# Kernel optimization log

Measured on AMD Instinct MI355X. Metric: run time of the kernel, lower is better.

## Reference

```python
import jax, jax.numpy as jnp
import numpy as np

L, N, EMB, H = 4, 50000, 128, 4
R, HID, LBL = 16, 64, 32
E = 625000


def setup_inputs() -> dict:
    key = jax.random.key(0)
    ks = jax.random.split(key, 10)
    s = 0.05
    return {
        "embedding": jax.random.normal(ks[0], (L, N, EMB), jnp.float32),
        "in_proj_w": jax.random.normal(ks[1], (3 * EMB, EMB), jnp.float32) * s,
        "in_proj_b": jnp.zeros((3 * EMB,), jnp.float32),
        "out_proj_w": jax.random.normal(ks[2], (EMB, EMB), jnp.float32) * s,
        "out_proj_b": jnp.zeros((EMB,), jnp.float32),
        "w1": jax.random.normal(ks[3], (R, EMB, HID), jnp.float32) * s,
        "root1": jax.random.normal(ks[4], (EMB, HID), jnp.float32) * s,
        "b1": jnp.zeros((HID,), jnp.float32),
        "w2": jax.random.normal(ks[5], (R, HID, LBL), jnp.float32) * s,
        "root2": jax.random.normal(ks[6], (HID, LBL), jnp.float32) * s,
        "b2": jnp.zeros((LBL,), jnp.float32),
        "edge_index": jax.random.randint(ks[7], (2, E), 0, N, dtype=jnp.int64),
        "edge_type": jax.random.randint(ks[8], (E,), 0, R, dtype=jnp.int64),
    }


def mha_self(x, wi, bi, wo, bo):
    # x: (L, N, EMB) -- torch nn.MultiheadAttention, batch_first=False, q=k=v=x
    Ls, Ns, Es = x.shape
    hd = Es // H
    qkv = x @ wi.T + bi                      # (L, N, 3E)
    q, k, v = jnp.split(qkv, 3, axis=-1)
    q = q.reshape(Ls, Ns, H, hd)
    k = k.reshape(Ls, Ns, H, hd)
    v = v.reshape(Ls, Ns, H, hd)
    scores = jnp.einsum('lnhd,mnhd->nhlm', q, k) / np.sqrt(hd).astype(np.float32)
    attn = jax.nn.softmax(scores, axis=-1)
    out = jnp.einsum('nhlm,mnhd->lnhd', attn, v).reshape(Ls, Ns, Es)
    return out @ wo.T + bo


def rgcn_layer(x, src, dst, etype, W, root, bias):
    # PyG RGCNConv (num_bases=None, aggr='mean'):
    # out[n] = x[n] @ root + bias + sum_r mean_{e: dst=n, type=r} x[src_e] @ W[r]
    Rr, fin, fout = W.shape
    seg = etype * N + dst                                   # (E,) combined (rel, dst)
    msg_sum = jax.ops.segment_sum(x[src], seg, num_segments=Rr * N)   # (R*N, fin)
    cnt = jax.ops.segment_sum(jnp.ones((src.shape[0],), x.dtype), seg,
                              num_segments=Rr * N)
    mean = (msg_sum / jnp.maximum(cnt, 1.0)[:, None]).reshape(Rr, N, fin)
    agg = jnp.einsum('rni,rio->no', mean, W)                # per-relation GEMM
    return agg + x @ root + bias


def reference(embedding, in_proj_w, in_proj_b, out_proj_w, out_proj_b,
              w1, root1, b1, w2, root2, b2, edge_index, edge_type):
    attn_out = mha_self(embedding, in_proj_w, in_proj_b, out_proj_w, out_proj_b)
    x = attn_out[0]                                         # (N, EMB)
    src, dst = edge_index[0], edge_index[1]
    x = jax.nn.relu(rgcn_layer(x, src, dst, edge_type, w1, root1, b1))
    x = rgcn_layer(x, src, dst, edge_type, w2, root2, b2)
    return jax.nn.softmax(x, axis=-1)
```

## Files before the change

### kernel.cpp

```cpp
#include <hip/hip_runtime.h>
#include <hip/hip_bf16.h>
#include <math.h>

#define NNODES 50000
#define NEDGE 625000
#define RREL 16
#define SCAN_NB 196

typedef __attribute__((ext_vector_type(8))) short short8;
typedef __attribute__((ext_vector_type(4))) float f32x4;

__device__ __forceinline__ float bfu(ushort u) {
  return __uint_as_float(((unsigned)u) << 16);
}
__device__ __forceinline__ ushort f2b(float f) {
  __hip_bfloat16 h = __float2bfloat16(f);
  return *(ushort*)&h;
}

__global__ __launch_bounds__(256) void prep_weights(
    const float* __restrict__ ipw, const float* __restrict__ opw,
    const float* __restrict__ w1, const float* __restrict__ root1,
    const float* __restrict__ w2, const float* __restrict__ root2,
    __hip_bfloat16* __restrict__ BTqkv, __hip_bfloat16* __restrict__ BTout,
    __hip_bfloat16* __restrict__ BT1, __hip_bfloat16* __restrict__ BT2) {
  int i = blockIdx.x * 256 + threadIdx.x;
  if (i < 49152) {
    BTqkv[i] = __float2bfloat16(ipw[i]);
  } else if (i < 65536) {
    int j = i - 49152;
    BTout[j] = __float2bfloat16(opw[j]);
  } else if (i < 65536 + 139264) {
    int j = i - 65536; int c = j / 128, k = j % 128;
    float v;
    if (c < 64) v = root1[k * 64 + c];
    else { int r = (c - 64) >> 6, o = (c - 64) & 63; v = w1[r * 8192 + k * 64 + o]; }
    BT1[j] = __float2bfloat16(v);
  } else if (i < 65536 + 139264 + 34816) {
    int j = i - 65536 - 139264; int c = j / 64, k = j % 64;
    float v;
    if (c < 32) v = root2[k * 32 + c];
    else { int r = (c - 32) >> 5, o = (c - 32) & 31; v = w2[r * 2048 + k * 32 + o]; }
    BT2[j] = __float2bfloat16(v);
  }
}

__global__ __launch_bounds__(256) void qkv_gemm(
    const float* __restrict__ A, const __hip_bfloat16* __restrict__ BT,
    const float* __restrict__ bias, __hip_bfloat16* __restrict__ C) {
  __shared__ ushort As[128 * 128];
  __shared__ ushort Cs[128 * 136];
  const int t = threadIdx.x;
  const long row0 = (long)blockIdx.x * 128;

#pragma unroll
  for (int c = t; c < 128 * 16; c += 256) {
    int r = c >> 4, cc = c & 15;
    long gm = row0 + r;
    int4 v = make_int4(0, 0, 0, 0);
    if (gm < 200000) {
      const float* ap = A + gm * 128 + cc * 8;
      float4 f0 = *(const float4*)ap;
      float4 f1 = *(const float4*)(ap + 4);
      v.x = (int)f2b(f0.x) | ((int)f2b(f0.y) << 16);
      v.y = (int)f2b(f0.z) | ((int)f2b(f0.w) << 16);
      v.z = (int)f2b(f1.x) | ((int)f2b(f1.y) << 16);
      v.w = (int)f2b(f1.z) | ((int)f2b(f1.w) << 16);
    }
    *(int4*)(As + r * 128 + ((cc ^ (r & 7)) * 8)) = v;
  }
  __syncthreads();

  const int lane = t & 63, w = t >> 6;
  const int wr = (w >> 1) * 64, wc = (w & 1) * 64;
  const int lrow = lane & 15, lk = lane >> 4;
  const int nstrips = (row0 < NNODES) ? 3 : 2;

  for (int s = 0; s < nstrips; s++) {
    const int col0 = (s == 2) ? 0 : 128 + s * 128;
    const long Meff = (s == 2) ? NNODES : 200000;

    const ushort* bp[4];
#pragma unroll
    for (int j = 0; j < 4; j++)
      bp[j] = (const ushort*)BT + (long)(col0 + wc + j * 16 + lrow) * 128 + lk * 8;

    f32x4 acc[4][4];
#pragma unroll
    for (int i = 0; i < 4; i++)
#pragma unroll
      for (int j = 0; j < 4; j++) acc[i][j] = (f32x4){0.f, 0.f, 0.f, 0.f};

#pragma unroll
    for (int k0 = 0; k0 < 128; k0 += 32) {
      const int cb = k0 / 8 + lk;
      short8 af[4], bfr[4];
#pragma unroll
      for (int j = 0; j < 4; j++) bfr[j] = *(const short8*)(bp[j] + k0);
#pragma unroll
      for (int i = 0; i < 4; i++) {
        int ra = wr + i * 16 + lrow;
        af[i] = *(const short8*)(As + ra * 128 + ((cb ^ (ra & 7)) * 8));
      }
#pragma unroll
      for (int i = 0; i < 4; i++)
#pragma unroll
        for (int j = 0; j < 4; j++)
          acc[i][j] = __builtin_amdgcn_mfma_f32_16x16x32_bf16(af[i], bfr[j], acc[i][j], 0, 0, 0);
    }

    __syncthreads();
#pragma unroll
    for (int j = 0; j < 4; j++) {
      int coll = wc + j * 16 + lrow;
      float bv = bias[col0 + coll];
#pragma unroll
      for (int i = 0; i < 4; i++) {
        int rbase = wr + i * 16 + lk * 4;
#pragma unroll
        for (int q = 0; q < 4; q++)
          Cs[(rbase + q) * 136 + coll] = f2b(acc[i][j][q] + bv);
      }
    }
    __syncthreads();
#pragma unroll
    for (int idx = t; idx < 128 * 16; idx += 256) {
      int r = idx >> 4, k = idx & 15;
      long gm = row0 + r;
      if (gm < Meff)
        *(int4*)((ushort*)C + gm * 384 + col0 + k * 8) = *(const int4*)(Cs + r * 136 + k * 8);
    }
  }
}

template <int K, bool AF32>
__global__ __launch_bounds__(256) void gemm_mfma(
    const void* __restrict__ Av, const __hip_bfloat16* __restrict__ BT,
    const float* __restrict__ bias, __hip_bfloat16* __restrict__ C,
    int M, int N, int lda, int ldc) {
  constexpr int CPR = K / 8;
  __shared__ ushort smem[128 * 136];
  ushort* As = smem;
  const int t = threadIdx.x;
  const long row0 = (long)blockIdx.x * 128;
  const int col0 = blockIdx.y * 128;
  if (row0 >= M) return;

#pragma unroll
  for (int c = t; c < 128 * CPR; c += 256) {
    int r = c / CPR, cc = c % CPR;
    long gm = row0 + r;
    int4 v = make_int4(0, 0, 0, 0);
    if (gm < M) {
      if constexpr (AF32) {
        const float* ap = (const float*)Av + gm * lda + cc * 8;
        float4 f0 = *(const float4*)ap;
        float4 f1 = *(const float4*)(ap + 4);
        v.x = (int)f2b(f0.x) | ((int)f2b(f0.y) << 16);
        v.y = (int)f2b(f0.z) | ((int)f2b(f0.w) << 16);
        v.z = (int)f2b(f1.x) | ((int)f2b(f1.y) << 16);
        v.w = (int)f2b(f1.z) | ((int)f2b(f1.w) << 16);
      } else {
        v = *(const int4*)((const ushort*)Av + gm * lda + cc * 8);
      }
    }
    *(int4*)(As + r * K + ((cc ^ (r & 7)) * 8)) = v;
  }
  __syncthreads();

  const int lane = t & 63, w = t >> 6;
  const int wr = (w >> 1) * 64, wc = (w & 1) * 64;
  const int lrow = lane & 15, lk = lane >> 4;

  const ushort* bp[4];
#pragma unroll
  for (int j = 0; j < 4; j++) {
    int gn = col0 + wc + j * 16 + lrow;
    if (gn > N - 1) gn = N - 1;
    bp[j] = (const ushort*)BT + (long)gn * K + lk * 8;
  }

  f32x4 acc[4][4];
#pragma unroll
  for (int i = 0; i < 4; i++)
#pragma unroll
    for (int j = 0; j < 4; j++) acc[i][j] = (f32x4){0.f, 0.f, 0.f, 0.f};

#pragma unroll
  for (int k0 = 0; k0 < K; k0 += 32) {
    const int cb = k0 / 8 + lk;
    short8 af[4], bfr[4];
#pragma unroll
    for (int j = 0; j < 4; j++) bfr[j] = *(const short8*)(bp[j] + k0);
#pragma unroll
    for (int i = 0; i < 4; i++) {
      int ra = wr + i * 16 + lrow;
      af[i] = *(const short8*)(As + ra * K + ((cb ^ (ra & 7)) * 8));
    }
#pragma unroll
    for (int i = 0; i < 4; i++)
#pragma unroll
      for (int j = 0; j < 4; j++)
        acc[i][j] = __builtin_amdgcn_mfma_f32_16x16x32_bf16(af[i], bfr[j], acc[i][j], 0, 0, 0);
  }

  __syncthreads();
  ushort* Cs = smem;
#pragma unroll
  for (int j = 0; j < 4; j++) {
    int coll = wc + j * 16 + lrow;
    int bc = col0 + coll; if (bc > N - 1) bc = N - 1;
    float bv = bias ? bias[bc] : 0.f;
#pragma unroll
    for (int i = 0; i < 4; i++) {
      int rbase = wr + i * 16 + lk * 4;
#pragma unroll
      for (int q = 0; q < 4; q++)
        Cs[(rbase + q) * 136 + coll] = f2b(acc[i][j][q] + bv);
    }
  }
  __syncthreads();
#pragma unroll
  for (int idx = t; idx < 128 * 16; idx += 256) {
    int r = idx >> 4, k = idx & 15;
    long gm = row0 + r;
    int col = col0 + k * 8;
    if (gm < M && col < N)
      *(int4*)((ushort*)C + gm * ldc + col) = *(const int4*)(Cs + r * 136 + k * 8);
  }
}

__global__ __launch_bounds__(256) void attn_kernel(
    const __hip_bfloat16* __restrict__ qkv, __hip_bfloat16* __restrict__ o0) {
  int t = threadIdx.x;
  int n = blockIdx.x * 2 + (t >> 7);
  int ch = t & 127;
  float q = __bfloat162float(qkv[(size_t)n * 384 + ch]);
  float s[4];
#pragma unroll
  for (int m = 0; m < 4; m++) {
    float kk = __bfloat162float(qkv[(size_t)(m * NNODES + n) * 384 + 128 + ch]);
    float p = q * kk;
#pragma unroll
    for (int off = 16; off; off >>= 1) p += __shfl_xor(p, off);
    s[m] = p * 0.17677669529663687f;
  }
  float mx = fmaxf(fmaxf(s[0], s[1]), fmaxf(s[2], s[3]));
  float e[4], sum = 0.f;
#pragma unroll
  for (int m = 0; m < 4; m++) { e[m] = __expf(s[m] - mx); sum += e[m]; }
  float inv = 1.0f / sum;
  float out = 0.f;
#pragma unroll
  for (int m = 0; m < 4; m++)
    out += e[m] * inv * __bfloat162float(qkv[(size_t)(m * NNODES + n) * 384 + 256 + ch]);
  o0[(size_t)n * 128 + ch] = __float2bfloat16(out);
}

__global__ __launch_bounds__(256) void count_edges(
    const int* __restrict__ dst, const int* __restrict__ et, int* __restrict__ cnt) {
  int e = blockIdx.x * 256 + threadIdx.x;
  if (e < NEDGE) atomicAdd(&cnt[et[e] * NNODES + dst[e]], 1);
}

__global__ __launch_bounds__(256) void scan1(
    const int* __restrict__ cnt, int* __restrict__ off, int* __restrict__ part) {
  int t = threadIdx.x, b = blockIdx.x;
  int i = b * 256 + t;
  int v = 0;
  if (i < NNODES) {
#pragma unroll
    for (int r = 0; r < RREL; r++) v += cnt[r * NNODES + i];
  }
  __shared__ int sm[256];
  sm[t] = v;
  __syncthreads();
#pragma unroll
  for (int o = 1; o < 256; o <<= 1) {
    int x = (t >= o) ? sm[t - o] : 0;
    __syncthreads();
    sm[t] += x;
    __syncthreads();
  }
  if (i < NNODES) off[i] = sm[t] - v;
  if (t == 255) part[b] = sm[t];
}

__global__ __launch_bounds__(256) void scan2(int* __restrict__ part) {
  int t = threadIdx.x;
  int v = (t < SCAN_NB) ? part[t] : 0;
  __shared__ int sm[256];
  sm[t] = v;
  __syncthreads();
#pragma unroll
  for (int o = 1; o < 256; o <<= 1) {
    int x = (t >= o) ? sm[t - o] : 0;
    __syncthreads();
    sm[t] += x;
    __syncthreads();
  }
  if (t < SCAN_NB) part[t] = sm[t] - v;
}

__global__ __launch_bounds__(256) void scan3(int* __restrict__ off, const int* __restrict__ part) {
  int i = blockIdx.x * 256 + threadIdx.x;
  if (i < NNODES) off[i] += part[blockIdx.x];
  if (i == 0) off[NNODES] = NEDGE;
}

__global__ __launch_bounds__(256) void scatter_edges(
    const int* __restrict__ src, const int* __restrict__ dst, const int* __restrict__ et,
    const int* __restrict__ cnt, const int* __restrict__ off,
    int* __restrict__ fill, unsigned* __restrict__ sorted, float* __restrict__ scales) {
  int e = blockIdx.x * 256 + threadIdx.x;
  if (e >= NEDGE) return;
  int d = dst[e], r = et[e], s = src[e];
  int pos = off[d] + atomicAdd(&fill[d], 1);
  sorted[pos] = (unsigned)s | ((unsigned)r << 16);
  scales[pos] = 1.0f / (float)cnt[r * NNODES + d];
}

__global__ __launch_bounds__(256) void fused1(
    const int* __restrict__ off, const unsigned* __restrict__ sorted,
    const float* __restrict__ scales, const ushort* __restrict__ Y1,
    const float* __restrict__ b1, __hip_bfloat16* __restrict__ x1b) {
  int w = threadIdx.x >> 6, lane = threadIdx.x & 63;
  int d = blockIdx.x * 4 + w;
  int s0 = off[d], s1 = off[d + 1];
  float acc = bfu(Y1[(size_t)d * 1088 + lane]) + b1[lane];
  for (int i = s0; i < s1; i++) {
    unsigned p = sorted[i];
    acc += bfu(Y1[(size_t)(p & 0xFFFF) * 1088 + 64 + (p >> 16) * 64 + lane]) * scales[i];
  }
  x1b[(size_t)d * 64 + lane] = __float2bfloat16(fmaxf(acc, 0.f));
}

__global__ __launch_bounds__(256) void fused2(
    const int* __restrict__ off, const unsigned* __restrict__ sorted,
    const float* __restrict__ scales, const ushort* __restrict__ Y2,
    const float* __restrict__ b2, float* __restrict__ out) {
  int w = threadIdx.x >> 6, lane = threadIdx.x & 63;
  int d = blockIdx.x * 4 + w;
  int j = lane & 31, half = lane >> 5;
  int s0 = off[d], s1 = off[d + 1];
  float acc = 0.f;
  for (int i = s0 + half; i < s1; i += 2) {
    unsigned p = sorted[i];
    acc += bfu(Y2[(size_t)(p & 0xFFFF) * 544 + 32 + (p >> 16) * 32 + j]) * scales[i];
  }
  acc += __shfl_xor(acc, 32);
  float v = acc + bfu(Y2[(size_t)d * 544 + j]) + b2[j];
  float mx = v;
#pragma unroll
  for (int o = 16; o; o >>= 1) mx = fmaxf(mx, __shfl_xor(mx, o));
  float e = __expf(v - mx);
  float sum = e;
#pragma unroll
  for (int o = 16; o; o >>= 1) sum += __shfl_xor(sum, o);
  if (half == 0) out[(size_t)d * 32 + j] = e / sum;
}

extern "C" void kernel_launch(void* const* d_in, const int* in_sizes, int n_in,
                              void* d_out, int out_size, void* d_ws, size_t ws_size,
                              hipStream_t stream) {
  (void)in_sizes; (void)n_in; (void)out_size; (void)ws_size;
  const float* emb   = (const float*)d_in[0];
  const float* ipw   = (const float*)d_in[1];
  const float* ipb   = (const float*)d_in[2];
  const float* opw   = (const float*)d_in[3];
  const float* opb   = (const float*)d_in[4];
  const float* w1    = (const float*)d_in[5];
  const float* root1 = (const float*)d_in[6];
  const float* b1    = (const float*)d_in[7];
  const float* w2    = (const float*)d_in[8];
  const float* root2 = (const float*)d_in[9];
  const float* b2    = (const float*)d_in[10];
  const int*   eidx  = (const int*)d_in[11];
  const int*   etype = (const int*)d_in[12];
  const int* srcp = eidx;
  const int* dstp = eidx + NEDGE;

  unsigned char* ws = (unsigned char*)d_ws;
  size_t off_b = 0;
  auto alloc = [&](size_t bytes) {
    unsigned char* p = ws + off_b;
    off_b += (bytes + 255) & ~(size_t)255;
    return p;
  };

  unsigned char* R = alloc(153600000);
  __hip_bfloat16* qkv = (__hip_bfloat16*)R;
  __hip_bfloat16* Y1  = (__hip_bfloat16*)R;
  __hip_bfloat16* Y2  = (__hip_bfloat16*)R;
  __hip_bfloat16* o0  = (__hip_bfloat16*)alloc(12800000);
  __hip_bfloat16* x0  = (__hip_bfloat16*)alloc(12800000);
  __hip_bfloat16* x1b = (__hip_bfloat16*)alloc(6400000);
  int*            cnt = (int*)alloc(3200000);
  int*            offs = (int*)alloc((NNODES + 1) * 4);
  int*            fill = (int*)alloc(NNODES * 4);
  int*            part = (int*)alloc(SCAN_NB * 4);
  unsigned*       sorted = (unsigned*)alloc(NEDGE * 4);
  float*          scales = (float*)alloc(NEDGE * 4);
  __hip_bfloat16* BTqkv = (__hip_bfloat16*)alloc(98304);
  __hip_bfloat16* BTout = (__hip_bfloat16*)alloc(32768);
  __hip_bfloat16* BT1   = (__hip_bfloat16*)alloc(278528);
  __hip_bfloat16* BT2   = (__hip_bfloat16*)alloc(69632);

  prep_weights<<<dim3((241664 + 255) / 256), dim3(256), 0, stream>>>(
      ipw, opw, w1, root1, w2, root2, BTqkv, BTout, BT1, BT2);
  hipMemsetAsync(cnt, 0, (size_t)RREL * NNODES * sizeof(int), stream);
  hipMemsetAsync(fill, 0, (size_t)NNODES * sizeof(int), stream);
  count_edges<<<dim3((NEDGE + 255) / 256), dim3(256), 0, stream>>>(dstp, etype, cnt);
  scan1<<<dim3(SCAN_NB), dim3(256), 0, stream>>>(cnt, offs, part);
  scan2<<<dim3(1), dim3(256), 0, stream>>>(part);
  scan3<<<dim3(SCAN_NB), dim3(256), 0, stream>>>(offs, part);
  scatter_edges<<<dim3((NEDGE + 255) / 256), dim3(256), 0, stream>>>(
      srcp, dstp, etype, cnt, offs, fill, sorted, scales);

  qkv_gemm<<<dim3(1563), dim3(256), 0, stream>>>(emb, BTqkv, ipb, qkv);

  attn_kernel<<<dim3(25000), dim3(256), 0, stream>>>(qkv, o0);

  gemm_mfma<128, false><<<dim3(391, 1), dim3(256), 0, stream>>>(
      o0, BTout, opb, x0, NNODES, 128, 128, 128);

  gemm_mfma<128, false><<<dim3(391, 9), dim3(256), 0, stream>>>(
      x0, BT1, nullptr, Y1, NNODES, 1088, 128, 1088);

  fused1<<<dim3(NNODES / 4), dim3(256), 0, stream>>>(
      offs, sorted, scales, (const ushort*)Y1, b1, x1b);

  gemm_mfma<64, false><<<dim3(391, 5), dim3(256), 0, stream>>>(
      x1b, BT2, nullptr, Y2, NNODES, 544, 64, 544);

  fused2<<<dim3(NNODES / 4), dim3(256), 0, stream>>>(
      offs, sorted, scales, (const ushort*)Y2, b2, (float*)d_out);
}
```

Before: 371.3 us.

## Loop column strips per block to reuse A tile, shrink epilogue LDS, widen attention loads

The GEMM kernel now keeps a 128-row A tile in LDS and loops over several 128-column output strips within one block, so each A tile is loaded once per group of strips instead of once per column block. The epilogue stages the output through a half-size LDS buffer in two passes. That lowers LDS use and may raise occupancy, at the cost of extra barriers. The attention kernel now handles one node per wavefront with two channels per lane, using 32-bit loads and a shorter shuffle reduction.

```diff
diff --git a/kernel.cpp b/kernel.cpp
--- a/kernel.cpp
+++ b/kernel.cpp
@@ -45,11 +45,39 @@
   }
 }
 
+#define EPILOGUE_STORE(MEFF, NCOLS, LDC, BIASEXPR)                              \
+  for (int p = 0; p < 2; p++) {                                                 \
+    __syncthreads();                                                            \
+    if ((w >> 1) == p) {                                                        \
+      _Pragma("unroll")                                                         \
+      for (int j = 0; j < 4; j++) {                                             \
+        int coll = wc + j * 16 + lrow;                                          \
+        float bv = (BIASEXPR);                                                  \
+        _Pragma("unroll")                                                       \
+        for (int i = 0; i < 4; i++) {                                           \
+          int rloc = i * 16 + lk * 4;                                           \
+          _Pragma("unroll")                                                     \
+          for (int q = 0; q < 4; q++)                                           \
+            Cs[(rloc + q) * 132 + coll] = f2b(acc[i][j][q] + bv);               \
+        }                                                                       \
+      }                                                                         \
+    }                                                                           \
+    __syncthreads();                                                            \
+    _Pragma("unroll")                                                           \
+    for (int idx = t; idx < 64 * 16; idx += 256) {                              \
+      int r = idx >> 4, k = idx & 15;                                           \
+      long gm = row0 + p * 64 + r;                                              \
+      int col = col0 + k * 8;                                                   \
+      if (gm < (MEFF) && col < (NCOLS))                                         \
+        *(int4*)((ushort*)C + gm * (LDC) + col) = *(const int4*)(Cs + r * 132 + k * 8); \
+    }                                                                           \
+  }
+
 __global__ __launch_bounds__(256) void qkv_gemm(
     const float* __restrict__ A, const __hip_bfloat16* __restrict__ BT,
     const float* __restrict__ bias, __hip_bfloat16* __restrict__ C) {
   __shared__ ushort As[128 * 128];
-  __shared__ ushort Cs[128 * 136];
+  __shared__ ushort Cs[64 * 132];
   const int t = threadIdx.x;
   const long row0 = (long)blockIdx.x * 128;
 
@@ -109,61 +137,27 @@
           acc[i][j] = __builtin_amdgcn_mfma_f32_16x16x32_bf16(af[i], bfr[j], acc[i][j], 0, 0, 0);
     }
 
-    __syncthreads();
-#pragma unroll
-    for (int j = 0; j < 4; j++) {
-      int coll = wc + j * 16 + lrow;
-      float bv = bias[col0 + coll];
-#pragma unroll
-      for (int i = 0; i < 4; i++) {
-        int rbase = wr + i * 16 + lk * 4;
-#pragma unroll
-        for (int q = 0; q < 4; q++)
-          Cs[(rbase + q) * 136 + coll] = f2b(acc[i][j][q] + bv);
-      }
-    }
-    __syncthreads();
-#pragma unroll
-    for (int idx = t; idx < 128 * 16; idx += 256) {
-      int r = idx >> 4, k = idx & 15;
-      long gm = row0 + r;
-      if (gm < Meff)
-        *(int4*)((ushort*)C + gm * 384 + col0 + k * 8) = *(const int4*)(Cs + r * 136 + k * 8);
-    }
-  }
-}
-
-template <int K, bool AF32>
-__global__ __launch_bounds__(256) void gemm_mfma(
-    const void* __restrict__ Av, const __hip_bfloat16* __restrict__ BT,
+    EPILOGUE_STORE(Meff, 384, 384, bias[col0 + coll])
+  }
+}
+
+template <int K>
+__global__ __launch_bounds__(256) void gemm_strips(
+    const __hip_bfloat16* __restrict__ Av, const __hip_bfloat16* __restrict__ BT,
     const float* __restrict__ bias, __hip_bfloat16* __restrict__ C,
-    int M, int N, int lda, int ldc) {
+    int M, int N, int ldc, int spg) {
   constexpr int CPR = K / 8;
-  __shared__ ushort smem[128 * 136];
-  ushort* As = smem;
+  __shared__ ushort As[128 * K];
+  __shared__ ushort Cs[64 * 132];
   const int t = threadIdx.x;
   const long row0 = (long)blockIdx.x * 128;
-  const int col0 = blockIdx.y * 128;
-  if (row0 >= M) return;
 
 #pragma unroll
   for (int c = t; c < 128 * CPR; c += 256) {
     int r = c / CPR, cc = c % CPR;
     long gm = row0 + r;
     int4 v = make_int4(0, 0, 0, 0);
-    if (gm < M) {
-      if constexpr (AF32) {
-        const float* ap = (const float*)Av + gm * lda + cc * 8;
-        float4 f0 = *(const float4*)ap;
-        float4 f1 = *(const float4*)(ap + 4);
-        v.x = (int)f2b(f0.x) | ((int)f2b(f0.y) << 16);
-        v.y = (int)f2b(f0.z) | ((int)f2b(f0.w) << 16);
-        v.z = (int)f2b(f1.x) | ((int)f2b(f1.y) << 16);
-        v.w = (int)f2b(f1.z) | ((int)f2b(f1.w) << 16);
-      } else {
-        v = *(const int4*)((const ushort*)Av + gm * lda + cc * 8);
-      }
-    }
+    if (gm < M) v = *(const int4*)((const ushort*)Av + gm * K + cc * 8);
     *(int4*)(As + r * K + ((cc ^ (r & 7)) * 8)) = v;
   }
   __syncthreads();
@@ -171,78 +165,63 @@
   const int lane = t & 63, w = t >> 6;
   const int wr = (w >> 1) * 64, wc = (w & 1) * 64;
   const int lrow = lane & 15, lk = lane >> 4;
-
-  const ushort* bp[4];
-#pragma unroll
-  for (int j = 0; j < 4; j++) {
-    int gn = col0 + wc + j * 16 + lrow;
-    if (gn > N - 1) gn = N - 1;
-    bp[j] = (const ushort*)BT + (long)gn * K + lk * 8;
-  }
-
-  f32x4 acc[4][4];
-#pragma unroll
-  for (int i = 0; i < 4; i++)
-#pragma unroll
-    for (int j = 0; j < 4; j++) acc[i][j] = (f32x4){0.f, 0.f, 0.f, 0.f};
-
-#pragma unroll
-  for (int k0 = 0; k0 < K; k0 += 32) {
-    const int cb = k0 / 8 + lk;
-    short8 af[4], bfr[4];
-#pragma unroll
-    for (int j = 0; j < 4; j++) bfr[j] = *(const short8*)(bp[j] + k0);
-#pragma unroll
-    for (int i = 0; i < 4; i++) {
-      int ra = wr + i * 16 + lrow;
-      af[i] = *(const short8*)(As + ra * K + ((cb ^ (ra & 7)) * 8));
+  const int nstrips = (N + 127) / 128;
+  const int sbeg = blockIdx.y * spg;
+  const int send = min(sbeg + spg, nstrips);
+
+  for (int s = sbeg; s < send; s++) {
+    const int col0 = s * 128;
+
+    const ushort* bp[4];
+#pragma unroll
+    for (int j = 0; j < 4; j++) {
+      int gn = col0 + wc + j * 16 + lrow;
+      if (gn > N - 1) gn = N - 1;
+      bp[j] = (const ushort*)BT + (long)gn * K + lk * 8;
     }
+
+    f32x4 acc[4][4];
 #pragma unroll
     for (int i = 0; i < 4; i++)
 #pragma unroll
-      for (int j = 0; j < 4; j++)
-        acc[i][j] = __builtin_amdgcn_mfma_f32_16x16x32_bf16(af[i], bfr[j], acc[i][j], 0, 0, 0);
-  }
-
-  __syncthreads();
-  ushort* Cs = smem;
-#pragma unroll
-  for (int j = 0; j < 4; j++) {
-    int coll = wc + j * 16 + lrow;
-    int bc = col0 + coll; if (bc > N - 1) bc = N - 1;
-    float bv = bias ? bias[bc] : 0.f;
-#pragma unroll
-    for (int i = 0; i < 4; i++) {
-      int rbase = wr + i * 16 + lk * 4;
-#pragma unroll
-      for (int q = 0; q < 4; q++)
-        Cs[(rbase + q) * 136 + coll] = f2b(acc[i][j][q] + bv);
+      for (int j = 0; j < 4; j++) acc[i][j] = (f32x4){0.f, 0.f, 0.f, 0.f};
+
+#pragma unroll
+    for (int k0 = 0; k0 < K; k0 += 32) {
+      const int cb = k0 / 8 + lk;
+      short8 af[4], bfr[4];
+#pragma unroll
+      for (int j = 0; j < 4; j++) bfr[j] = *(const short8*)(bp[j] + k0);
+#pragma unroll
+      for (int i = 0; i < 4; i++) {
+        int ra = wr + i * 16 + lrow;
+        af[i] = *(const short8*)(As + ra * K + ((cb ^ (ra & 7)) * 8));
+      }
+#pragma unroll
+      for (int i = 0; i < 4; i++)
+#pragma unroll
+        for (int j = 0; j < 4; j++)
+          acc[i][j] = __builtin_amdgcn_mfma_f32_16x16x32_bf16(af[i], bfr[j], acc[i][j], 0, 0, 0);
     }
-  }
-  __syncthreads();
-#pragma unroll
-  for (int idx = t; idx < 128 * 16; idx += 256) {
-    int r = idx >> 4, k = idx & 15;
-    long gm = row0 + r;
-    int col = col0 + k * 8;
-    if (gm < M && col < N)
-      *(int4*)((ushort*)C + gm * ldc + col) = *(const int4*)(Cs + r * 136 + k * 8);
+
+    EPILOGUE_STORE(M, N, ldc, bias ? bias[min(col0 + coll, N - 1)] : 0.f)
   }
 }
 
 __global__ __launch_bounds__(256) void attn_kernel(
     const __hip_bfloat16* __restrict__ qkv, __hip_bfloat16* __restrict__ o0) {
-  int t = threadIdx.x;
-  int n = blockIdx.x * 2 + (t >> 7);
-  int ch = t & 127;
-  float q = __bfloat162float(qkv[(size_t)n * 384 + ch]);
+  int w = threadIdx.x >> 6, lane = threadIdx.x & 63;
+  int n = blockIdx.x * 4 + w;
+  const ushort* base = (const ushort*)qkv;
+  uint qv = *(const uint*)(base + (size_t)n * 384 + lane * 2);
+  float q0 = bfu(qv & 0xffff), q1 = bfu(qv >> 16);
   float s[4];
 #pragma unroll
   for (int m = 0; m < 4; m++) {
-    float kk = __bfloat162float(qkv[(size_t)(m * NNODES + n) * 384 + 128 + ch]);
-    float p = q * kk;
-#pragma unroll
-    for (int off = 16; off; off >>= 1) p += __shfl_xor(p, off);
+    uint kk = *(const uint*)(base + (size_t)(m * NNODES + n) * 384 + 128 + lane * 2);
+    float p = q0 * bfu(kk & 0xffff) + q1 * bfu(kk >> 16);
+#pragma unroll
+    for (int off = 8; off; off >>= 1) p += __shfl_xor(p, off);
     s[m] = p * 0.17677669529663687f;
   }
   float mx = fmaxf(fmaxf(s[0], s[1]), fmaxf(s[2], s[3]));
@@ -250,11 +229,15 @@
 #pragma unroll
   for (int m = 0; m < 4; m++) { e[m] = __expf(s[m] - mx); sum += e[m]; }
   float inv = 1.0f / sum;
-  float out = 0.f;
-#pragma unroll
-  for (int m = 0; m < 4; m++)
-    out += e[m] * inv * __bfloat162float(qkv[(size_t)(m * NNODES + n) * 384 + 256 + ch]);
-  o0[(size_t)n * 128 + ch] = __float2bfloat16(out);
+  float o0f = 0.f, o1f = 0.f;
+#pragma unroll
+  for (int m = 0; m < 4; m++) {
+    uint vv = *(const uint*)(base + (size_t)(m * NNODES + n) * 384 + 256 + lane * 2);
+    float wgt = e[m] * inv;
+    o0f += wgt * bfu(vv & 0xffff);
+    o1f += wgt * bfu(vv >> 16);
+  }
+  *(uint*)((ushort*)o0 + (size_t)n * 128 + lane * 2) = (uint)f2b(o0f) | ((uint)f2b(o1f) << 16);
 }
 
 __global__ __launch_bounds__(256) void count_edges(
@@ -419,19 +402,19 @@
 
   qkv_gemm<<<dim3(1563), dim3(256), 0, stream>>>(emb, BTqkv, ipb, qkv);
 
-  attn_kernel<<<dim3(25000), dim3(256), 0, stream>>>(qkv, o0);
-
-  gemm_mfma<128, false><<<dim3(391, 1), dim3(256), 0, stream>>>(
-      o0, BTout, opb, x0, NNODES, 128, 128, 128);
-
-  gemm_mfma<128, false><<<dim3(391, 9), dim3(256), 0, stream>>>(
-      x0, BT1, nullptr, Y1, NNODES, 1088, 128, 1088);
+  attn_kernel<<<dim3(12500), dim3(256), 0, stream>>>(qkv, o0);
+
+  gemm_strips<128><<<dim3(391, 1), dim3(256), 0, stream>>>(
+      o0, BTout, opb, x0, NNODES, 128, 128, 1);
+
+  gemm_strips<128><<<dim3(391, 3), dim3(256), 0, stream>>>(
+      x0, BT1, nullptr, Y1, NNODES, 1088, 1088, 3);
 
   fused1<<<dim3(NNODES / 4), dim3(256), 0, stream>>>(
       offs, sorted, scales, (const ushort*)Y1, b1, x1b);
 
-  gemm_mfma<64, false><<<dim3(391, 5), dim3(256), 0, stream>>>(
-      x1b, BT2, nullptr, Y2, NNODES, 544, 64, 544);
+  gemm_strips<64><<<dim3(391, 2), dim3(256), 0, stream>>>(
+      x1b, BT2, nullptr, Y2, NNODES, 544, 544, 3);
 
   fused2<<<dim3(NNODES / 4), dim3(256), 0, stream>>>(
       offs, sorted, scales, (const ushort*)Y2, b2, (float*)d_out);
```

Result: slower. 385.4 us (+3.8%).
